# Kernel optimization log

Measured on AMD Instinct MI355X. Metric: run time of the kernel, lower is better.

## Reference

```python
import math
import jax, jax.numpy as jnp
import numpy as np

B, N, E, R = 1024, 200, 256, 256

def _layernorm(x, g, b, eps=1e-5):
    mu = x.mean(-1, keepdims=True)
    var = ((x - mu) ** 2).mean(-1, keepdims=True)
    return (x - mu) / jnp.sqrt(var + eps) * g + b

def setup_inputs() -> dict:
    key = jax.random.key(0)
    ks = jax.random.split(key, 16)
    d = {}
    d["e_emb"] = jax.random.normal(ks[0], (B, E), jnp.float32)
    d["nb_rel"] = jax.random.normal(ks[1], (B, N, R), jnp.float32)
    d["delta_t"] = jax.random.uniform(ks[2], (B, N), jnp.float32) * 10.0
    d["r_emb"] = jax.random.normal(ks[3], (B, R), jnp.float32)
    d["hist_mask"] = jax.random.randint(ks[4], (B, N), 0, 2).astype(bool)
    d["rel_w"] = jax.random.normal(ks[5], (E, R), jnp.float32) / math.sqrt(R)
    d["log_tau1"] = jnp.asarray(1.0, jnp.float32)
    d["log_tau2"] = jnp.asarray(2.5, jnp.float32)
    d["sharpness"] = jnp.asarray(1.5, jnp.float32)
    d["log_gamma"] = jnp.asarray(-2.0, jnp.float32)
    d["attn_w"] = jax.random.normal(ks[6], (3, E, E), jnp.float32) / math.sqrt(E)
    d["sp_w"] = jax.random.normal(ks[7], (3, E, 6 * E), jnp.float32) / math.sqrt(6 * E)
    d["sp_b"] = jnp.zeros((3, E), jnp.float32)
    d["ln_g"] = jnp.ones((3, E), jnp.float32)
    d["ln_b"] = jnp.zeros((3, E), jnp.float32)
    d["csq_w"] = jax.random.normal(ks[8], (E, R), jnp.float32) / math.sqrt(R)
    d["csq_b"] = jnp.zeros((E,), jnp.float32)
    d["csl_w"] = jax.random.normal(ks[9], (3, E), jnp.float32) / math.sqrt(E)
    d["csl_b"] = jnp.zeros((3,), jnp.float32)
    d["on_g"] = jnp.ones((E,), jnp.float32)
    d["on_b"] = jnp.zeros((E,), jnp.float32)
    return d

def _pna_one_scale(msgs, mask, e_emb, q_key, attn_w, sp_w, sp_b, ln_g, ln_b):
    # msgs: [B,N,E], mask: [B,N] bool, e_emb: [B,E], q_key: [B,E]
    valid_f = mask[..., None].astype(msgs.dtype)
    n_valid = jnp.maximum(mask.astype(msgs.dtype).sum(1, keepdims=True), 1.0)  # [B,1]
    msgs_v = msgs * valid_f
    mean_v = msgs_v.sum(1) / n_valid
    max_v = msgs_v.max(1)
    min_v = jnp.clip(jnp.where(mask[..., None], msgs, 10000.0).min(1), -10000.0, 10000.0)
    sq_m = (jnp.clip(msgs_v, -10.0, 10.0) ** 2).sum(1) / n_valid
    std_v = jnp.sqrt(jnp.maximum(sq_m - mean_v ** 2, 1e-6))
    q_proj = q_key @ attn_w.T  # [B,E]
    attn_raw = jnp.einsum('bne,be->bn', msgs, q_proj) / math.sqrt(msgs.shape[-1])
    attn_raw = jnp.where(mask, attn_raw, -10000.0)
    all_invalid = ~mask.any(1, keepdims=True)  # [B,1]
    attn_raw = jnp.where(all_invalid, 0.0, attn_raw)
    attn_p = jax.nn.softmax(attn_raw, axis=-1)
    attn_v = jnp.einsum('bn,bne->be', attn_p, msgs)
    feats = jnp.concatenate([mean_v, max_v, min_v, std_v, attn_v, e_emb], axis=-1)  # [B,6E]
    h = feats @ sp_w.T + sp_b
    h = _layernorm(h, ln_g, ln_b)
    return jax.nn.gelu(h, approximate=False)  # dropout = identity (eval mode)

def reference(e_emb, nb_rel, delta_t, r_emb, hist_mask, rel_w, log_tau1, log_tau2,
              sharpness, log_gamma, attn_w, sp_w, sp_b, ln_g, ln_b,
              csq_w, csq_b, csl_w, csl_b, on_g, on_b):
    msgs = jnp.einsum('bnr,er->bne', nb_rel, rel_w)
    gamma = jnp.exp(log_gamma)
    decay = jnp.exp(-gamma * jnp.maximum(delta_t, 0.0))
    msgs_dec = msgs * decay[..., None]
    tau1 = jnp.exp(log_tau1)
    tau2 = jnp.exp(log_tau2) + tau1
    sharp = jnp.clip(sharpness, 0.1, 5.0)
    w_fine = jax.nn.sigmoid(-sharp * (delta_t - tau1))
    w_coarse = jax.nn.sigmoid(sharp * (delta_t - tau2))
    w_mid = jnp.maximum(1.0 - w_fine - w_coarse, 0.0)
    scale_w = jnp.stack([w_fine, w_mid, w_coarse])  # [3,B,N]
    m_scales = msgs_dec[None] * scale_w[..., None]  # [3,B,N,E]
    q_key = r_emb @ rel_w.T  # [B,E]
    pna_v = jax.vmap(_pna_one_scale, in_axes=(0, None, None, None, 0, 0, 0, 0, 0))
    scales = pna_v(m_scales, hist_mask, e_emb, q_key, attn_w, sp_w, sp_b, ln_g, ln_b)  # [3,B,E]
    sq = r_emb @ csq_w.T + csq_b  # [B,E]
    logits = sq @ csl_w.T + csl_b  # [B,3]
    weights = jax.nn.softmax(logits, axis=-1)
    out = jnp.einsum('bs,sbe->be', weights, scales)
    return _layernorm(out, on_g, on_b)  # drop = identity (eval)
```

## Files before the change

kernel.cpp:

```cpp
#include <hip/hip_runtime.h>
#include <math.h>

#define B_   1024
#define N_   200
#define NR_  208
#define NT_  13
#define E_   256
#define R_   256
#define K6_  1536

typedef __attribute__((ext_vector_type(8))) short bf16x8;
typedef __attribute__((ext_vector_type(4))) float f32x4;

__device__ __forceinline__ unsigned short f2bf(float f) {
  unsigned int u = __float_as_uint(f);
  u += 0x7fffu + ((u >> 16) & 1u);
  return (unsigned short)(u >> 16);
}

__device__ __forceinline__ float gelu_exact(float x) {
  return 0.5f * x * (1.f + erff(x * 0.70710678118654752f));
}

__global__ __launch_bounds__(256) void k_cast(const float* __restrict__ rel_w,
                                              const float* __restrict__ sp_w,
                                              unsigned short* __restrict__ rw_bf,
                                              unsigned short* __restrict__ spw_bf) {
  int idx = blockIdx.x * 256 + threadIdx.x;
  if (idx < E_ * R_) rw_bf[idx] = f2bf(rel_w[idx]);
  int j = idx - E_ * R_;
  if (j >= 0 && j < 3 * E_ * K6_) spw_bf[j] = f2bf(sp_w[j]);
}

__global__ __launch_bounds__(256) void k_prep(
    const float* __restrict__ r_emb, const float* __restrict__ rel_w,
    const float* __restrict__ csq_w, const float* __restrict__ csq_b,
    const float* __restrict__ csl_w, const float* __restrict__ csl_b,
    const float* __restrict__ attn_w,
    float* __restrict__ t_ws, float* __restrict__ wts) {
  __shared__ __align__(16) float re[4][256];
  __shared__ __align__(16) float qk[4][256];
  __shared__ __align__(16) float sqs[4][256];
  __shared__ __align__(16) float qp[3][4][256];
  __shared__ float lg[4][3];
  int b0 = blockIdx.x * 4;
  int tid = threadIdx.x;
  int e = tid;
#pragma unroll
  for (int i = 0; i < 4; ++i)
    re[i][tid] = r_emb[(size_t)(b0 + i) * 256 + tid];
  __syncthreads();
  {
    float qkv[4], sv[4];
#pragma unroll
    for (int i = 0; i < 4; ++i) { qkv[i] = 0.f; sv[i] = 0.f; }
    const float4* w4 = (const float4*)(rel_w) + (size_t)e * 64;
    const float4* c4 = (const float4*)(csq_w) + (size_t)e * 64;
    for (int r = 0; r < 64; ++r) {
      float4 w = w4[r];
      float4 c = c4[r];
#pragma unroll
      for (int i = 0; i < 4; ++i) {
        float4 x = ((const float4*)re[i])[r];
        qkv[i] += w.x * x.x + w.y * x.y + w.z * x.z + w.w * x.w;
        sv[i] += c.x * x.x + c.y * x.y + c.z * x.z + c.w * x.w;
      }
    }
    float cb = csq_b[e];
#pragma unroll
    for (int i = 0; i < 4; ++i) {
      qk[i][e] = qkv[i];
      sqs[i][e] = sv[i] + cb;
    }
  }
  __syncthreads();
  if (tid < 12) {
    int i = tid / 3, k = tid % 3;
    float acc = csl_b[k];
    for (int ee = 0; ee < 256; ++ee) acc += sqs[i][ee] * csl_w[k * 256 + ee];
    lg[i][k] = acc;
  }
  __syncthreads();
  if (tid < 4) {
    float l0 = lg[tid][0], l1 = lg[tid][1], l2 = lg[tid][2];
    float m = fmaxf(l0, fmaxf(l1, l2));
    float e0 = expf(l0 - m), e1 = expf(l1 - m), e2 = expf(l2 - m);
    float inv = 1.f / (e0 + e1 + e2);
    wts[(b0 + tid) * 4 + 0] = e0 * inv;
    wts[(b0 + tid) * 4 + 1] = e1 * inv;
    wts[(b0 + tid) * 4 + 2] = e2 * inv;
  }
  {
    float qpv[3][4];
#pragma unroll
    for (int s = 0; s < 3; ++s)
#pragma unroll
      for (int i = 0; i < 4; ++i) qpv[s][i] = 0.f;
#pragma unroll
    for (int s = 0; s < 3; ++s) {
      const float4* a4 = (const float4*)(attn_w) + ((size_t)s * 256 + e) * 64;
      for (int r = 0; r < 64; ++r) {
        float4 w = a4[r];
#pragma unroll
        for (int i = 0; i < 4; ++i) {
          float4 x = ((const float4*)qk[i])[r];
          qpv[s][i] += w.x * x.x + w.y * x.y + w.z * x.z + w.w * x.w;
        }
      }
    }
    __syncthreads();
#pragma unroll
    for (int s = 0; s < 3; ++s)
#pragma unroll
      for (int i = 0; i < 4; ++i) qp[s][i][e] = qpv[s][i];
  }
  __syncthreads();
  {
    int r = tid;
    float tacc[3][4];
#pragma unroll
    for (int s = 0; s < 3; ++s)
#pragma unroll
      for (int i = 0; i < 4; ++i) tacc[s][i] = 0.f;
    for (int e4 = 0; e4 < 64; ++e4) {
      float4 qv[3][4];
#pragma unroll
      for (int s = 0; s < 3; ++s)
#pragma unroll
        for (int i = 0; i < 4; ++i)
          qv[s][i] = ((const float4*)qp[s][i])[e4];
#pragma unroll
      for (int j = 0; j < 4; ++j) {
        float w = rel_w[(size_t)(e4 * 4 + j) * 256 + r];
#pragma unroll
        for (int s = 0; s < 3; ++s)
#pragma unroll
          for (int i = 0; i < 4; ++i) {
            float q = (j == 0) ? qv[s][i].x : (j == 1) ? qv[s][i].y
                      : (j == 2) ? qv[s][i].z : qv[s][i].w;
            tacc[s][i] = fmaf(q, w, tacc[s][i]);
          }
      }
    }
#pragma unroll
    for (int s = 0; s < 3; ++s)
#pragma unroll
      for (int i = 0; i < 4; ++i)
        t_ws[((size_t)s * B_ + b0 + i) * 256 + r] = tacc[s][i];
  }
}

__global__ __launch_bounds__(1024, 4) void k1_main(
    const float* __restrict__ nb_rel, const float* __restrict__ delta_t,
    const unsigned char* __restrict__ hm_raw, const float* __restrict__ e_emb,
    const float* __restrict__ p_lt1, const float* __restrict__ p_lt2,
    const float* __restrict__ p_sh, const float* __restrict__ p_lgm,
    const unsigned short* __restrict__ rw_bf, const float* __restrict__ t_ws,
    unsigned short* __restrict__ feats) {
  __shared__ __align__(16) struct {
    unsigned int a[NR_ * 132];
    float araw[3][NR_];
    float c[3][NR_];
    float p[3][NR_];
    float nmeta[NR_][9];
  } sm;
  int b = blockIdx.x;
  int tid = threadIdx.x;
  int lane = tid & 63, wave = tid >> 6;
  int row16 = lane & 15, quad = lane >> 4;

  float4 tf0 = *(const float4*)&t_ws[((size_t)0 * B_ + b) * 256 + lane * 4];
  float4 tf1 = *(const float4*)&t_ws[((size_t)1 * B_ + b) * 256 + lane * 4];
  float4 tf2 = *(const float4*)&t_ws[((size_t)2 * B_ + b) * 256 + lane * 4];

  int hasNZoff = 0, hasFP = 0;
  {
    unsigned char cc = hm_raw[tid];
    if ((tid & 3) != 0 && cc != 0) {
      hasNZoff = 1;
      if (cc == 0x3Fu || cc == 0x80u) hasFP = 1;
    }
  }
  int cntNZ = __syncthreads_count(hasNZoff);
  int cntFP = __syncthreads_count(hasFP);
  int mmode = (cntNZ == 0) ? 0 : (cntFP > 0 ? 2 : 1);

  float tau1 = expf(p_lt1[0]);
  float tau2 = expf(p_lt2[0]) + tau1;
  float sharp = fminf(fmaxf(p_sh[0], 0.1f), 5.0f);
  float gamma = expf(p_lgm[0]);

  bool mk = false;
  if (tid < NR_) {
    float mf = 0.f, c0 = 0.f, c1 = 0.f, c2 = 0.f;
    if (tid < N_) {
      size_t mi = (size_t)b * N_ + tid;
      if (mmode == 0)      mk = ((const int*)hm_raw)[mi] != 0;
      else if (mmode == 1) mk = hm_raw[mi] != 0;
      else                 mk = ((const float*)hm_raw)[mi] != 0.f;
      float dt = delta_t[mi];
      mf = mk ? 1.f : 0.f;
      float decay = expf(-gamma * fmaxf(dt, 0.f));
      float wf = 1.f / (1.f + expf(sharp * (dt - tau1)));
      float wc = 1.f / (1.f + expf(-sharp * (dt - tau2)));
      float wm = fmaxf(1.f - wf - wc, 0.f);
      c0 = decay * wf; c1 = decay * wm; c2 = decay * wc;
    }
    sm.c[0][tid] = c0; sm.c[1][tid] = c1; sm.c[2][tid] = c2;
    sm.nmeta[tid][0] = mf * c0;
    sm.nmeta[tid][1] = mf * c1;
    sm.nmeta[tid][2] = mf * c2;
    sm.nmeta[tid][3] = mk ? 0.f : 1e4f;
    sm.nmeta[tid][7] = mf;
  }
  int cnt = __syncthreads_count(mk ? 1 : 0);
  float nvf = fmaxf((float)cnt, 1.f);
  bool allinv = (cnt == 0);

  {
    const float* src = nb_rel + (size_t)b * N_ * 256;
    float4 x = *(const float4*)(src + (size_t)wave * 256 + lane * 4);
    for (int i = 0; i < NT_; ++i) {
      int ncur = i * 16 + wave;
      float4 xn;
      if (i < NT_ - 1) {
        int nn = (i + 1) * 16 + wave;
        int gn = (nn < N_) ? nn : (N_ - 1);
        xn = *(const float4*)(src + (size_t)gn * 256 + lane * 4);
      }
      float d0 = x.x * tf0.x + x.y * tf0.y + x.z * tf0.z + x.w * tf0.w;
      float d1 = x.x * tf1.x + x.y * tf1.y + x.z * tf1.z + x.w * tf1.w;
      float d2 = x.x * tf2.x + x.y * tf2.y + x.z * tf2.z + x.w * tf2.w;
#pragma unroll
      for (int o = 1; o < 64; o <<= 1) {
        d0 += __shfl_xor(d0, o, 64);
        d1 += __shfl_xor(d1, o, 64);
        d2 += __shfl_xor(d2, o, 64);
      }
      if (lane < 3) sm.araw[lane][ncur] = (lane == 0) ? d0 : ((lane == 1) ? d1 : d2);
      uint2 pk;
      pk.x = (unsigned int)f2bf(x.x) | ((unsigned int)f2bf(x.y) << 16);
      pk.y = (unsigned int)f2bf(x.z) | ((unsigned int)f2bf(x.w) << 16);
      *(uint2*)&sm.a[ncur * 132 + lane * 2] = pk;
      x = xn;
    }
  }

  bf16x8 bfr[8];
  {
    int e = wave * 16 + row16;
#pragma unroll
    for (int ks = 0; ks < 8; ++ks)
      bfr[ks] = *(const bf16x8*)(rw_bf + (size_t)e * 256 + ks * 32 + quad * 8);
  }
  __syncthreads();

  if (tid < NR_) {
    float l0 = -1e30f, l1 = -1e30f, l2 = -1e30f;
    if (tid < N_) {
      bool mkk = sm.nmeta[tid][7] > 0.5f;
      l0 = sm.c[0][tid] * sm.araw[0][tid] * 0.0625f;
      l1 = sm.c[1][tid] * sm.araw[1][tid] * 0.0625f;
      l2 = sm.c[2][tid] * sm.araw[2][tid] * 0.0625f;
      l0 = mkk ? l0 : -1e4f; l1 = mkk ? l1 : -1e4f; l2 = mkk ? l2 : -1e4f;
      if (allinv) { l0 = 0.f; l1 = 0.f; l2 = 0.f; }
    }
    sm.p[0][tid] = l0; sm.p[1][tid] = l1; sm.p[2][tid] = l2;
  }
  __syncthreads();

  if (wave < 3) {
    int s = wave;
    float m = -1e30f;
    for (int n = lane; n < NR_; n += 64) m = fmaxf(m, sm.p[s][n]);
#pragma unroll
    for (int o = 32; o >= 1; o >>= 1) m = fmaxf(m, __shfl_xor(m, o, 64));
    float ssum = 0.f;
    for (int n = lane; n < NR_; n += 64) ssum += expf(sm.p[s][n] - m);
#pragma unroll
    for (int o = 32; o >= 1; o >>= 1) ssum += __shfl_xor(ssum, o, 64);
    float inv = 1.f / ssum;
    for (int n = lane; n < NR_; n += 64) {
      float pv = expf(sm.p[s][n] - m) * inv;
      sm.nmeta[n][4 + s] = pv * sm.c[s][n];
    }
  } else if (wave == 3) {
    for (int i = lane; i < 256; i += 64) {
      unsigned short v = f2bf(e_emb[(size_t)b * 256 + i]);
      feats[((size_t)0 * B_ + b) * K6_ + 1280 + i] = v;
      feats[((size_t)1 * B_ + b) * K6_ + 1280 + i] = v;
      feats[((size_t)2 * B_ + b) * K6_ + 1280 + i] = v;
    }
  }
  __syncthreads();

  float s_mean[3], s_mx[3], s_mn[3], s_sq[3], s_av[3];
#pragma unroll
  for (int s = 0; s < 3; ++s) {
    s_mean[s] = 0.f; s_mx[s] = -1e30f; s_mn[s] = 1e30f;
    s_sq[s] = 0.f; s_av[s] = 0.f;
  }

  for (int nt = 0; nt < NT_; ++nt) {
    f32x4 acc;
#pragma unroll
    for (int cc = 0; cc < 4; ++cc) acc[cc] = 0.f;
#pragma unroll
    for (int ks = 0; ks < 8; ++ks) {
      bf16x8 af = *(const bf16x8*)&sm.a[(nt * 16 + row16) * 132 + ks * 16 + quad * 4];
      acc = __builtin_amdgcn_mfma_f32_16x16x32_bf16(af, bfr[ks], acc, 0, 0, 0);
    }
    int nb = nt * 16 + quad * 4;
#pragma unroll
    for (int rg = 0; rg < 4; ++rg) {
      int n = nb + rg;
      float cm0 = sm.nmeta[n][0], cm1 = sm.nmeta[n][1], cm2 = sm.nmeta[n][2];
      float off = sm.nmeta[n][3];
      float q0 = sm.nmeta[n][4], q1 = sm.nmeta[n][5], q2 = sm.nmeta[n][6];
      float m = acc[rg];
      float cmv[3] = {cm0, cm1, cm2};
      float qv[3] = {q0, q1, q2};
#pragma unroll
      for (int s = 0; s < 3; ++s) {
        float vm = cmv[s] * m;
        s_mean[s] += vm;
        s_mx[s] = fmaxf(s_mx[s], vm);
        s_mn[s] = fminf(s_mn[s], fmaf(cmv[s], m, off));
        float cv = fminf(fmaxf(vm, -10.f), 10.f);
        s_sq[s] = fmaf(cv, cv, s_sq[s]);
        s_av[s] = fmaf(qv[s], m, s_av[s]);
      }
    }
  }

#pragma unroll
  for (int s = 0; s < 3; ++s) {
    float vmean = s_mean[s];
    vmean += __shfl_xor(vmean, 16, 64); vmean += __shfl_xor(vmean, 32, 64);
    float vmx = s_mx[s];
    vmx = fmaxf(vmx, __shfl_xor(vmx, 16, 64)); vmx = fmaxf(vmx, __shfl_xor(vmx, 32, 64));
    float vmn = s_mn[s];
    vmn = fminf(vmn, __shfl_xor(vmn, 16, 64)); vmn = fminf(vmn, __shfl_xor(vmn, 32, 64));
    float vsq = s_sq[s];
    vsq += __shfl_xor(vsq, 16, 64); vsq += __shfl_xor(vsq, 32, 64);
    float vav = s_av[s];
    vav += __shfl_xor(vav, 16, 64); vav += __shfl_xor(vav, 32, 64);
    if (lane < 16) {
      int e = wave * 16 + lane;
      size_t base = ((size_t)s * B_ + b) * K6_;
      float meanv = vmean / nvf;
      float stdv = sqrtf(fmaxf(vsq / nvf - meanv * meanv, 1e-6f));
      float mnv = fminf(fmaxf(vmn, -1e4f), 1e4f);
      feats[base + e] = f2bf(meanv);
      feats[base + 256 + e] = f2bf(vmx);
      feats[base + 512 + e] = f2bf(mnv);
      feats[base + 768 + e] = f2bf(stdv);
      feats[base + 1024 + e] = f2bf(vav);
    }
  }
}

__global__ __launch_bounds__(256) void k2_kernel(
    const unsigned short* __restrict__ feats, const unsigned short* __restrict__ spw_bf,
    const float* __restrict__ sp_b, float* __restrict__ hbuf) {
  __shared__ __align__(16) unsigned int a[16 * 132];
  int id = blockIdx.x;
  int s = id >> 7;
  int rem = id & 127;
  int b0 = (rem >> 1) * 16;
  int e0 = (rem & 1) * 128;
  int tid = threadIdx.x, lane = tid & 63, wave = tid >> 6;
  int row16 = lane & 15, quad = lane >> 4;
  f32x4 acc[2];
#pragma unroll
  for (int t = 0; t < 2; ++t)
#pragma unroll
    for (int cc = 0; cc < 4; ++cc) acc[t][cc] = 0.f;

  for (int kc = 0; kc < 6; ++kc) {
    __syncthreads();
    for (int j = tid; j < 512; j += 256) {
      int rw = j >> 5, ck = j & 31;
      bf16x8 v = *(const bf16x8*)(feats + ((size_t)s * B_ + b0 + rw) * K6_ + kc * 256 + ck * 8);
      *(bf16x8*)((unsigned short*)&a[rw * 132] + ck * 8) = v;
    }
    __syncthreads();
#pragma unroll
    for (int ks = 0; ks < 8; ++ks) {
      bf16x8 af = *(const bf16x8*)&a[row16 * 132 + ks * 16 + quad * 4];
#pragma unroll
      for (int t = 0; t < 2; ++t) {
        int e = e0 + wave * 32 + t * 16 + row16;
        bf16x8 bfr = *(const bf16x8*)(spw_bf + ((size_t)s * E_ + e) * K6_ + kc * 256 + ks * 32 + quad * 8);
        acc[t] = __builtin_amdgcn_mfma_f32_16x16x32_bf16(af, bfr, acc[t], 0, 0, 0);
      }
    }
  }
#pragma unroll
  for (int t = 0; t < 2; ++t) {
    int e = e0 + wave * 32 + t * 16 + row16;
    float bias = sp_b[s * 256 + e];
#pragma unroll
    for (int rg = 0; rg < 4; ++rg) {
      int rw = quad * 4 + rg;
      hbuf[((size_t)s * B_ + b0 + rw) * 256 + e] = acc[t][rg] + bias;
    }
  }
}

__global__ __launch_bounds__(256) void k3_kernel(
    const float* __restrict__ hbuf, const float* __restrict__ wts,
    const float* __restrict__ ln_g, const float* __restrict__ ln_b,
    const float* __restrict__ on_g, const float* __restrict__ on_b,
    float* __restrict__ out) {
  __shared__ float rs[4], rq[4];
  int b = blockIdx.x, tid = threadIdx.x, lane = tid & 63, wave = tid >> 6;
  float o = 0.f;
#pragma unroll
  for (int s = 0; s < 3; ++s) {
    float h = hbuf[((size_t)s * B_ + b) * 256 + tid];
    float sum = h, sq = h * h;
#pragma unroll
    for (int off = 32; off >= 1; off >>= 1) {
      sum += __shfl_xor(sum, off, 64);
      sq += __shfl_xor(sq, off, 64);
    }
    if (lane == 0) { rs[wave] = sum; rq[wave] = sq; }
    __syncthreads();
    float ts = rs[0] + rs[1] + rs[2] + rs[3];
    float tq = rq[0] + rq[1] + rq[2] + rq[3];
    __syncthreads();
    float mu = ts * (1.f / 256.f);
    float var = tq * (1.f / 256.f) - mu * mu;
    float rstd = rsqrtf(var + 1e-5f);
    float v = (h - mu) * rstd * ln_g[s * 256 + tid] + ln_b[s * 256 + tid];
    o += wts[b * 4 + s] * gelu_exact(v);
  }
  float sum = o, sq = o * o;
#pragma unroll
  for (int off = 32; off >= 1; off >>= 1) {
    sum += __shfl_xor(sum, off, 64);
    sq += __shfl_xor(sq, off, 64);
  }
  if (lane == 0) { rs[wave] = sum; rq[wave] = sq; }
  __syncthreads();
  float ts = rs[0] + rs[1] + rs[2] + rs[3];
  float tq = rq[0] + rq[1] + rq[2] + rq[3];
  float mu = ts * (1.f / 256.f);
  float var = tq * (1.f / 256.f) - mu * mu;
  float rstd = rsqrtf(var + 1e-5f);
  out[(size_t)b * 256 + tid] = (o - mu) * rstd * on_g[tid] + on_b[tid];
}

extern "C" void kernel_launch(void* const* d_in, const int* in_sizes, int n_in,
                              void* d_out, int out_size, void* d_ws, size_t ws_size,
                              hipStream_t stream) {
  const float* e_emb   = (const float*)d_in[0];
  const float* nb_rel  = (const float*)d_in[1];
  const float* delta_t = (const float*)d_in[2];
  const float* r_emb   = (const float*)d_in[3];
  const unsigned char* hist_mask = (const unsigned char*)d_in[4];
  const float* rel_w   = (const float*)d_in[5];
  const float* lt1     = (const float*)d_in[6];
  const float* lt2     = (const float*)d_in[7];
  const float* shp     = (const float*)d_in[8];
  const float* lgm     = (const float*)d_in[9];
  const float* attn_w  = (const float*)d_in[10];
  const float* sp_w    = (const float*)d_in[11];
  const float* sp_b    = (const float*)d_in[12];
  const float* ln_g    = (const float*)d_in[13];
  const float* ln_b    = (const float*)d_in[14];
  const float* csq_w   = (const float*)d_in[15];
  const float* csq_b   = (const float*)d_in[16];
  const float* csl_w   = (const float*)d_in[17];
  const float* csl_b   = (const float*)d_in[18];
  const float* on_g    = (const float*)d_in[19];
  const float* on_b    = (const float*)d_in[20];
  float* out = (float*)d_out;

  char* ws = (char*)d_ws;
  unsigned short* rw_bf  = (unsigned short*)(ws + 0);
  unsigned short* spw_bf = (unsigned short*)(ws + 131072);
  float* t_ws   = (float*)(ws + 2490368);
  float* wts    = (float*)(ws + 5636096);
  unsigned short* feats = (unsigned short*)(ws + 5652480);
  float* hbuf   = (float*)(ws + 15089664);

  hipLaunchKernelGGL(k_cast, dim3(4864), dim3(256), 0, stream, rel_w, sp_w, rw_bf, spw_bf);
  hipLaunchKernelGGL(k_prep, dim3(256), dim3(256), 0, stream, r_emb, rel_w, csq_w, csq_b,
                     csl_w, csl_b, attn_w, t_ws, wts);
  hipLaunchKernelGGL(k1_main, dim3(1024), dim3(1024), 0, stream, nb_rel, delta_t, hist_mask,
                     e_emb, lt1, lt2, shp, lgm, rw_bf, t_ws, feats);
  hipLaunchKernelGGL(k2_kernel, dim3(384), dim3(256), 0, stream, feats, spw_bf, sp_b, hbuf);
  hipLaunchKernelGGL(k3_kernel, dim3(1024), dim3(256), 0, stream, hbuf, wts, ln_g, ln_b,
                     on_g, on_b, out);
}
```

Measured before the change: 526.0 us.

## Compute attention logits with MFMA and batch nb_rel loads up front

```diff
diff --git a/kernel.cpp b/kernel.cpp
--- a/kernel.cpp
+++ b/kernel.cpp
@@ -159,19 +159,14 @@
     unsigned short* __restrict__ feats) {
   __shared__ __align__(16) struct {
     unsigned int a[NR_ * 132];
-    float araw[3][NR_];
     float c[3][NR_];
     float p[3][NR_];
-    float nmeta[NR_][9];
+    float nmeta[NR_ * 12];
   } sm;
   int b = blockIdx.x;
   int tid = threadIdx.x;
   int lane = tid & 63, wave = tid >> 6;
   int row16 = lane & 15, quad = lane >> 4;
-
-  float4 tf0 = *(const float4*)&t_ws[((size_t)0 * B_ + b) * 256 + lane * 4];
-  float4 tf1 = *(const float4*)&t_ws[((size_t)1 * B_ + b) * 256 + lane * 4];
-  float4 tf2 = *(const float4*)&t_ws[((size_t)2 * B_ + b) * 256 + lane * 4];
 
   int hasNZoff = 0, hasFP = 0;
   {
@@ -185,10 +180,10 @@
   int cntFP = __syncthreads_count(hasFP);
   int mmode = (cntNZ == 0) ? 0 : (cntFP > 0 ? 2 : 1);
 
-  float tau1 = expf(p_lt1[0]);
-  float tau2 = expf(p_lt2[0]) + tau1;
+  float tau1 = __expf(p_lt1[0]);
+  float tau2 = __expf(p_lt2[0]) + tau1;
   float sharp = fminf(fmaxf(p_sh[0], 0.1f), 5.0f);
-  float gamma = expf(p_lgm[0]);
+  float gamma = __expf(p_lgm[0]);
 
   bool mk = false;
   if (tid < NR_) {
@@ -200,18 +195,18 @@
       else                 mk = ((const float*)hm_raw)[mi] != 0.f;
       float dt = delta_t[mi];
       mf = mk ? 1.f : 0.f;
-      float decay = expf(-gamma * fmaxf(dt, 0.f));
-      float wf = 1.f / (1.f + expf(sharp * (dt - tau1)));
-      float wc = 1.f / (1.f + expf(-sharp * (dt - tau2)));
+      float decay = __expf(-gamma * fmaxf(dt, 0.f));
+      float wf = 1.f / (1.f + __expf(sharp * (dt - tau1)));
+      float wc = 1.f / (1.f + __expf(-sharp * (dt - tau2)));
       float wm = fmaxf(1.f - wf - wc, 0.f);
       c0 = decay * wf; c1 = decay * wm; c2 = decay * wc;
     }
     sm.c[0][tid] = c0; sm.c[1][tid] = c1; sm.c[2][tid] = c2;
-    sm.nmeta[tid][0] = mf * c0;
-    sm.nmeta[tid][1] = mf * c1;
-    sm.nmeta[tid][2] = mf * c2;
-    sm.nmeta[tid][3] = mk ? 0.f : 1e4f;
-    sm.nmeta[tid][7] = mf;
+    f32x4 w0, w1;
+    w0[0] = mf * c0; w0[1] = mf * c1; w0[2] = mf * c2; w0[3] = mk ? 0.f : 1e4f;
+    w1[0] = 0.f; w1[1] = 0.f; w1[2] = 0.f; w1[3] = mf;
+    *(f32x4*)&sm.nmeta[tid * 12]     = w0;
+    *(f32x4*)&sm.nmeta[tid * 12 + 4] = w1;
   }
   int cnt = __syncthreads_count(mk ? 1 : 0);
   float nvf = fmaxf((float)cnt, 1.f);
@@ -219,72 +214,57 @@
 
   {
     const float* src = nb_rel + (size_t)b * N_ * 256;
-    float4 x = *(const float4*)(src + (size_t)wave * 256 + lane * 4);
+    float4 xs[NT_];
+#pragma unroll
     for (int i = 0; i < NT_; ++i) {
-      int ncur = i * 16 + wave;
-      float4 xn;
-      if (i < NT_ - 1) {
-        int nn = (i + 1) * 16 + wave;
-        int gn = (nn < N_) ? nn : (N_ - 1);
-        xn = *(const float4*)(src + (size_t)gn * 256 + lane * 4);
-      }
-      float d0 = x.x * tf0.x + x.y * tf0.y + x.z * tf0.z + x.w * tf0.w;
-      float d1 = x.x * tf1.x + x.y * tf1.y + x.z * tf1.z + x.w * tf1.w;
-      float d2 = x.x * tf2.x + x.y * tf2.y + x.z * tf2.z + x.w * tf2.w;
-#pragma unroll
-      for (int o = 1; o < 64; o <<= 1) {
-        d0 += __shfl_xor(d0, o, 64);
-        d1 += __shfl_xor(d1, o, 64);
-        d2 += __shfl_xor(d2, o, 64);
-      }
-      if (lane < 3) sm.araw[lane][ncur] = (lane == 0) ? d0 : ((lane == 1) ? d1 : d2);
+      int n = i * 16 + wave;
+      int gn = (n < N_) ? n : (N_ - 1);
+      xs[i] = *(const float4*)(src + (size_t)gn * 256 + lane * 4);
+    }
+#pragma unroll
+    for (int i = 0; i < NT_; ++i) {
       uint2 pk;
-      pk.x = (unsigned int)f2bf(x.x) | ((unsigned int)f2bf(x.y) << 16);
-      pk.y = (unsigned int)f2bf(x.z) | ((unsigned int)f2bf(x.w) << 16);
-      *(uint2*)&sm.a[ncur * 132 + lane * 2] = pk;
-      x = xn;
-    }
-  }
-
-  bf16x8 bfr[8];
-  {
-    int e = wave * 16 + row16;
-#pragma unroll
-    for (int ks = 0; ks < 8; ++ks)
-      bfr[ks] = *(const bf16x8*)(rw_bf + (size_t)e * 256 + ks * 32 + quad * 8);
-  }
-  __syncthreads();
-
-  if (tid < NR_) {
-    float l0 = -1e30f, l1 = -1e30f, l2 = -1e30f;
-    if (tid < N_) {
-      bool mkk = sm.nmeta[tid][7] > 0.5f;
-      l0 = sm.c[0][tid] * sm.araw[0][tid] * 0.0625f;
-      l1 = sm.c[1][tid] * sm.araw[1][tid] * 0.0625f;
-      l2 = sm.c[2][tid] * sm.araw[2][tid] * 0.0625f;
-      l0 = mkk ? l0 : -1e4f; l1 = mkk ? l1 : -1e4f; l2 = mkk ? l2 : -1e4f;
-      if (allinv) { l0 = 0.f; l1 = 0.f; l2 = 0.f; }
-    }
-    sm.p[0][tid] = l0; sm.p[1][tid] = l1; sm.p[2][tid] = l2;
-  }
-  __syncthreads();
-
-  if (wave < 3) {
-    int s = wave;
-    float m = -1e30f;
-    for (int n = lane; n < NR_; n += 64) m = fmaxf(m, sm.p[s][n]);
-#pragma unroll
-    for (int o = 32; o >= 1; o >>= 1) m = fmaxf(m, __shfl_xor(m, o, 64));
-    float ssum = 0.f;
-    for (int n = lane; n < NR_; n += 64) ssum += expf(sm.p[s][n] - m);
-#pragma unroll
-    for (int o = 32; o >= 1; o >>= 1) ssum += __shfl_xor(ssum, o, 64);
-    float inv = 1.f / ssum;
-    for (int n = lane; n < NR_; n += 64) {
-      float pv = expf(sm.p[s][n] - m) * inv;
-      sm.nmeta[n][4 + s] = pv * sm.c[s][n];
-    }
-  } else if (wave == 3) {
+      pk.x = (unsigned int)f2bf(xs[i].x) | ((unsigned int)f2bf(xs[i].y) << 16);
+      pk.y = (unsigned int)f2bf(xs[i].z) | ((unsigned int)f2bf(xs[i].w) << 16);
+      *(uint2*)&sm.a[(i * 16 + wave) * 132 + lane * 2] = pk;
+    }
+  }
+  __syncthreads();
+
+  if (wave < NT_) {
+    bf16x8 tfrag[8];
+    const float* tp = t_ws + ((size_t)row16 * B_ + b) * 256;
+#pragma unroll
+    for (int ks = 0; ks < 8; ++ks) {
+      bf16x8 tv = {0, 0, 0, 0, 0, 0, 0, 0};
+      if (row16 < 3) {
+        const float* q = tp + ks * 32 + quad * 8;
+#pragma unroll
+        for (int j = 0; j < 8; ++j) tv[j] = (short)f2bf(q[j]);
+      }
+      tfrag[ks] = tv;
+    }
+    f32x4 acc;
+#pragma unroll
+    for (int cc = 0; cc < 4; ++cc) acc[cc] = 0.f;
+#pragma unroll
+    for (int ks = 0; ks < 8; ++ks) {
+      bf16x8 af = *(const bf16x8*)&sm.a[(wave * 16 + row16) * 132 + ks * 16 + quad * 4];
+      acc = __builtin_amdgcn_mfma_f32_16x16x32_bf16(af, tfrag[ks], acc, 0, 0, 0);
+    }
+    if (row16 < 3) {
+#pragma unroll
+      for (int rg = 0; rg < 4; ++rg) {
+        int n = wave * 16 + quad * 4 + rg;
+        float cw = sm.c[row16][n];
+        float mf = sm.nmeta[n * 12 + 7];
+        float l = cw * acc[rg] * 0.0625f;
+        l = (mf > 0.5f) ? l : -1e4f;
+        if (allinv) l = (n < N_) ? 0.f : -1e4f;
+        sm.p[row16][n] = l;
+      }
+    }
+  } else if (wave == NT_) {
     for (int i = lane; i < 256; i += 64) {
       unsigned short v = f2bf(e_emb[(size_t)b * 256 + i]);
       feats[((size_t)0 * B_ + b) * K6_ + 1280 + i] = v;
@@ -292,6 +272,34 @@
       feats[((size_t)2 * B_ + b) * K6_ + 1280 + i] = v;
     }
   }
+
+  bf16x8 bfr[8];
+  {
+    int e = wave * 16 + row16;
+#pragma unroll
+    for (int ks = 0; ks < 8; ++ks)
+      bfr[ks] = *(const bf16x8*)(rw_bf + (size_t)e * 256 + ks * 32 + quad * 8);
+  }
+  __syncthreads();
+
+  if (wave < 3) {
+    int s = wave;
+    float m = -1e30f;
+    for (int n = lane; n < NR_; n += 64) m = fmaxf(m, sm.p[s][n]);
+#pragma unroll
+    for (int o = 32; o >= 1; o >>= 1) m = fmaxf(m, __shfl_xor(m, o, 64));
+    float ssum = 0.f;
+    for (int n = lane; n < NR_; n += 64) {
+      float ev = __expf(sm.p[s][n] - m);
+      sm.p[s][n] = ev;
+      ssum += ev;
+    }
+#pragma unroll
+    for (int o = 32; o >= 1; o >>= 1) ssum += __shfl_xor(ssum, o, 64);
+    float inv = 1.f / ssum;
+    for (int n = lane; n < NR_; n += 64)
+      sm.nmeta[n * 12 + 4 + s] = sm.p[s][n] * inv * sm.c[s][n];
+  }
   __syncthreads();
 
   float s_mean[3], s_mx[3], s_mn[3], s_sq[3], s_av[3];
@@ -313,22 +321,19 @@
     int nb = nt * 16 + quad * 4;
 #pragma unroll
     for (int rg = 0; rg < 4; ++rg) {
-      int n = nb + rg;
-      float cm0 = sm.nmeta[n][0], cm1 = sm.nmeta[n][1], cm2 = sm.nmeta[n][2];
-      float off = sm.nmeta[n][3];
-      float q0 = sm.nmeta[n][4], q1 = sm.nmeta[n][5], q2 = sm.nmeta[n][6];
+      const float* nm = &sm.nmeta[(size_t)(nb + rg) * 12];
+      f32x4 w0 = *(const f32x4*)nm;
+      f32x4 w1 = *(const f32x4*)(nm + 4);
       float m = acc[rg];
-      float cmv[3] = {cm0, cm1, cm2};
-      float qv[3] = {q0, q1, q2};
 #pragma unroll
       for (int s = 0; s < 3; ++s) {
-        float vm = cmv[s] * m;
+        float vm = w0[s] * m;
         s_mean[s] += vm;
         s_mx[s] = fmaxf(s_mx[s], vm);
-        s_mn[s] = fminf(s_mn[s], fmaf(cmv[s], m, off));
+        s_mn[s] = fminf(s_mn[s], fmaf(w0[s], m, w0[3]));
         float cv = fminf(fmaxf(vm, -10.f), 10.f);
         s_sq[s] = fmaf(cv, cv, s_sq[s]);
-        s_av[s] = fmaf(qv[s], m, s_av[s]);
+        s_av[s] = fmaf(w1[s], m, s_av[s]);
       }
     }
   }
```

After: 524.9 us. Within noise of the previous version (-0.2%).
